# Kernel optimization log

Hardware: AMD Instinct MI355X
Metric: run time of the kernel (lower is better)

The kernel has to match this reference:

```python
import jax, jax.numpy as jnp
import numpy as np

SIGMA = 0.02
B, CC, H, W = 4, 21, 96, 96
C_LOW, C_HIGH = 3, 512
N = H * W


def _grid_edges(h, w):
    idx = np.arange(h * w).reshape(h, w)
    eh = np.stack([idx[:, :-1].ravel(), idx[:, 1:].ravel()], 1)
    ev = np.stack([idx[:-1, :].ravel(), idx[1:, :].ravel()], 1)
    return np.concatenate([eh, ev], 0)  # [E,2] 4-connected grid edges


def _mst_bfs(feat, h, w):
    # feat: [C,h,w] numpy. Kruskal MST with norm2 edge weights, then BFS from node 0.
    n = h * w
    edges = _grid_edges(h, w)
    f = feat.reshape(feat.shape[0], -1)
    wts = ((f[:, edges[:, 0]] - f[:, edges[:, 1]]) ** 2).sum(0)
    order = np.argsort(wts, kind='stable')
    uf = np.arange(n)

    def find(x):
        r = x
        while uf[r] != r:
            r = uf[r]
        while uf[x] != r:
            uf[x], x = r, uf[x]
        return r

    adj = [[] for _ in range(n)]
    cnt = 0
    for ei in order:
        a, b = int(edges[ei, 0]), int(edges[ei, 1])
        ra, rb = find(a), find(b)
        if ra != rb:
            uf[ra] = rb
            adj[a].append(b)
            adj[b].append(a)
            cnt += 1
            if cnt == n - 1:
                break
    parent = np.zeros(n, np.int64)
    seen = np.zeros(n, bool)
    seen[0] = True
    levels, frontier = [[0]], [0]
    while frontier:
        nxt = []
        for u in frontier:
            for v in adj[u]:
                if not seen[v]:
                    seen[v] = True
                    parent[v] = u
                    nxt.append(v)
        if nxt:
            levels.append(nxt)
        frontier = nxt
    return parent, levels


def _tree_arrays(embed):
    # Host-side MST + BFS level schedule (integer tree topology, non-differentiable).
    e = np.asarray(jax.device_get(embed)).astype(np.float64)
    bn = e.shape[0]
    parents, levels = [], []
    for b in range(bn):
        p, lv = _mst_bfs(e[b], H, W)
        parents.append(p)
        levels.append(lv)
    D = max(len(lv) for lv in levels)
    L = max(max(len(l) for l in lv) for lv in levels)
    nodes = np.full((bn, D, L), N, np.int32)  # index N = dummy sink node
    for b, lv in enumerate(levels):
        for d, l in enumerate(lv):
            nodes[b, d, :len(l)] = l
    par = np.stack(parents)
    par = np.concatenate([par, np.full((bn, 1), N)], 1).astype(np.int32)
    msk = np.ones((bn, N + 1), np.float32)
    msk[:, 0] = 0.0  # root has no parent edge
    msk[:, N] = 0.0  # dummy node
    return jnp.asarray(nodes), jnp.asarray(par), jnp.asarray(msk)


def _tree_filter(feat, embed, nodes, parent, wmask, sigma):
    # feat [B,C,N], embed [B,Ce,N]. O(N) two-pass (leaf->root, root->leaf) tree DP:
    # out_i = sum_j (prod_{e in path(i,j)} w_e) f_j / same-with-f=1
    bn, c, nn = feat.shape
    ez = jnp.pad(embed, ((0, 0), (0, 0), (0, 1)))  # add dummy column
    ep = jax.vmap(lambda e, p: e[:, p])(ez, parent)  # parent embedding [B,Ce,N+1]
    w = wmask * jnp.exp(-((ez - ep) ** 2).sum(1) / sigma)  # edge weight per node [B,N+1]
    fa = jnp.concatenate([feat, jnp.ones((bn, 1, nn), feat.dtype)], 1)  # append norm channel
    fa = jnp.pad(fa, ((0, 0), (0, 0), (0, 1)))  # [B,C+1,N+1]

    def one(a0, wv, par, lvls):
        def up(a, lvl):  # children before parents: subtree aggregation
            return a.at[:, par[lvl]].add(wv[lvl] * a[:, lvl]), None
        a, _ = jax.lax.scan(up, a0, lvls[::-1])

        def down(s, lvl):  # parents before children: whole-tree aggregation
            wl = wv[lvl]
            sv = a[:, lvl] + wl * (s[:, par[lvl]] - wl * a[:, lvl])
            return s.at[:, lvl].set(sv), None
        s, _ = jax.lax.scan(down, a, lvls)
        return s

    s = jax.vmap(one)(fa, w, parent, nodes)
    return s[:, :c, :nn] / s[:, c:, :nn]


def _nearest(x, h, w):
    hr, wr = x.shape[-2:]
    ri = jnp.arange(h) * hr // h
    ci = jnp.arange(w) * wr // w
    return x[..., ri[:, None], ci[None, :]]


def setup_inputs():
    key = jax.random.key(0)
    k1, k2, k3, k4 = jax.random.split(key, 4)
    preds = jax.random.normal(k1, (B, CC, H, W), jnp.float32)
    low_feats = jax.random.uniform(k2, (B, C_LOW, H, W), dtype=jnp.float32)
    high_feats = 0.03 * jax.random.normal(k3, (B, C_HIGH, H, W), jnp.float32)
    roi = (jax.random.uniform(k4, (B, 1, 2 * H, 2 * W)) > 0.5).astype(jnp.float32)
    return {'preds': preds, 'low_feats': low_feats, 'high_feats': high_feats,
            'unlabeled_ROIs': roi}


def reference(preds, low_feats, high_feats, unlabeled_ROIs):
    nodes_l, par_l, msk_l = _tree_arrays(low_feats)
    nodes_h, par_h, msk_h = _tree_arrays(high_feats)
    roi = _nearest(unlabeled_ROIs, H, W)
    n = roi.sum()
    prob = jax.nn.sigmoid(preds)
    lf = low_feats.reshape(B, C_LOW, N)
    hf = high_feats.reshape(B, C_HIGH, N)
    AS = _tree_filter(prob.reshape(B, CC, N), lf, nodes_l, par_l, msk_l, SIGMA)
    AS = _tree_filter(AS, hf, nodes_h, par_h, msk_h, 1.0)
    loss = (roi * jnp.abs(prob - AS.reshape(B, CC, H, W))).sum()
    return jnp.where(n > 0, loss / n, jnp.zeros_like(loss))
```

## Files before the change

### kernel.cpp

```cpp
#include <hip/hip_runtime.h>
#include <math.h>
#include <stdint.h>
#include <stddef.h>


namespace {
constexpr int Bn  = 4, Cc = 21, Hh = 96, Ww = 96;
constexpr int Nn  = Hh * Ww;
constexpr int EhE = Hh * (Ww - 1);
constexpr int Ne  = EhE + (Hh - 1) * Ww;
constexpr int Clow = 3, Chigh = 512;
constexpr int NCh = Cc + 1;
constexpr int MAXD = 2048;
constexpr int TL  = 2 * (Nn - 1);
constexpr int ESL = 18432;
constexpr int SEG = 19;
constexpr int NR  = (TL + SEG - 1) / SEG;
constexpr int MAXC = 4608;

constexpr size_t OFF_ACC  = 0;
constexpr size_t OFF_PROB = 256;
constexpr size_t OFF_S1   = OFF_PROB + (size_t)Bn * Cc * Nn * 4;
constexpr size_t OFF_S2   = OFF_S1   + (size_t)Bn * NCh * Nn * 4;
constexpr size_t OFF_EW   = OFF_S2   + (size_t)Bn * NCh * Nn * 4;
constexpr size_t OFF_ORD  = OFF_EW   + (size_t)8 * Ne * 8;
constexpr size_t OFF_PPOS = OFF_ORD  + (size_t)8 * Nn * 4;
constexpr size_t OFF_WGT  = OFF_PPOS + (size_t)8 * Nn * 2;
constexpr size_t OFF_LEV  = OFF_WGT  + (size_t)8 * Nn * 4;
constexpr size_t OFF_D    = OFF_LEV  + (size_t)8 * MAXD * 4;
constexpr size_t OFF_DIR  = OFF_D    + 256;
constexpr size_t OFF_CBW  = OFF_DIR  + (size_t)8 * Nn * 4;
constexpr size_t OFF_CBE  = OFF_CBW  + (size_t)8 * Nn * 8;
constexpr size_t OFF_OPP  = OFF_CBE  + (size_t)8 * Nn * 4;
constexpr size_t OFF_SGN  = OFF_OPP  + (size_t)8 * ESL * 2;
constexpr size_t OFF_PNF  = OFF_SGN  + (size_t)8 * ESL;
constexpr size_t OFF_RNK  = OFF_PNF  + (size_t)8 * Nn * 4;
constexpr size_t OFF_EL1  = OFF_ORD;
constexpr size_t OFF_EL2  = OFF_WGT;
}

__device__ __forceinline__ void edge_nodes(int e, int& a, int& b) {
    if (e < EhE) { int h = e / (Ww - 1), w = e - h * (Ww - 1); a = h * Ww + w; b = a + 1; }
    else { int e2 = e - EhE; int h = e2 / Ww, w = e2 - h * Ww; a = h * Ww + w; b = a + Ww; }
}
__device__ __forceinline__ int dir_delta(int d) {
    return (d == 0) ? 1 : (d == 1) ? -1 : (d == 2) ? Ww : -Ww;
}
__device__ __forceinline__ int edge_of(int u, int d) {
    int h = u / Ww, w = u - h * Ww;
    if (d == 0) return h * (Ww - 1) + w;
    if (d == 1) return h * (Ww - 1) + w - 1;
    if (d == 2) return EhE + u;
    return EhE + u - Ww;
}

__device__ __forceinline__ unsigned long long mkkey(double w, int e) {
    unsigned long long q = (unsigned long long)(w * 70368744177664.0);
    if (q >= (1ull << 49)) q = (1ull << 49) - 1;
    return (q << 15) | (unsigned)e;
}

__device__ __forceinline__ void compact_push(bool keep, int val, int* cnt,
                                             unsigned short* out, int lane) {
    unsigned long long m = __ballot(keep ? 1 : 0);
    if (m == 0ull) return;
    int leader = __ffsll((unsigned long long)m) - 1;
    int base = 0;
    if (lane == leader) base = atomicAdd(cnt, __popcll(m));
    base = __shfl(base, leader, 64);
    if (keep) {
        unsigned long long lower = m & ((1ull << lane) - 1ull);
        out[base + __popcll(lower)] = (unsigned short)val;
    }
}

__device__ __forceinline__ int scan1024s(int val, int tid, int* wsum) {
    __syncthreads();
    int lane = tid & 63, wv = tid >> 6;
    int x = val;
    #pragma unroll
    for (int off = 1; off < 64; off <<= 1) {
        int y = __shfl_up(x, off, 64);
        if (lane >= off) x += y;
    }
    if (lane == 63) wsum[wv] = x;
    __syncthreads();
    if (wv == 0) {
        int s2 = (lane < 16) ? wsum[lane] : 0;
        #pragma unroll
        for (int off = 1; off < 16; off <<= 1) {
            int y = __shfl_up(s2, off, 64);
            if (lane >= off) s2 += y;
        }
        if (lane < 16) wsum[lane] = s2;
    }
    __syncthreads();
    int base = (wv > 0) ? wsum[wv - 1] : 0;
    return x + base;
}

__device__ __forceinline__ int scan1024_incl(int val, int tid, int* b0, int* b1) {
    b0[tid] = val;
    __syncthreads();
    int* s = b0; int* d = b1;
    for (int off = 1; off < 1024; off <<= 1) {
        int x = s[tid];
        if (tid >= off) x += s[tid - off];
        d[tid] = x;
        __syncthreads();
        int* t = s; s = d; d = t;
    }
    return s[tid];
}

__global__ void k_init(const float* __restrict__ preds, float* __restrict__ prob,
                       double* __restrict__ acc) {
    int idx = blockIdx.x * blockDim.x + threadIdx.x;
    if (idx == 0) { acc[0] = 0.0; acc[1] = 0.0; }
    if (idx >= Bn * Cc * Nn) return;
    prob[idx] = 1.0f / (1.0f + expf(-preds[idx]));
}

__global__ void k_edgew(const float* __restrict__ feat, int C, double* __restrict__ ew) {
    int idx = blockIdx.x * blockDim.x + threadIdx.x;
    if (idx >= Bn * Ne) return;
    int b = idx / Ne, e = idx - b * Ne;
    int a, c2; edge_nodes(e, a, c2);
    const float* fa = feat + (size_t)b * C * Nn + a;
    const float* fb = feat + (size_t)b * C * Nn + c2;
    double s = 0.0;
    int c = 0;
    for (; c + 16 <= C; c += 16) {
        float va[16], vb[16];
        #pragma unroll
        for (int k = 0; k < 16; k++) {
            va[k] = fa[(size_t)(c + k) * Nn];
            vb[k] = fb[(size_t)(c + k) * Nn];
        }
        #pragma unroll
        for (int k = 0; k < 16; k++) {
            double d = (double)va[k] - (double)vb[k];
            s += d * d;
        }
    }
    for (; c < C; c++) {
        double d = (double)fa[(size_t)c * Nn] - (double)fb[(size_t)c * Nn];
        s += d * d;
    }
    ew[idx] = s;
}

__global__ void __launch_bounds__(1024)
k_mst(char* __restrict__ ws) {
    const int tb = blockIdx.x, tid = threadIdx.x;
    const int lane = tid & 63;
    const double* ew = (const double*)(ws + OFF_EW) + (size_t)tb * Ne;
    int* dirG = (int*)(ws + OFF_DIR) + (size_t)tb * Nn;
    unsigned short* elA = (unsigned short*)(ws + OFF_EL1) + (size_t)tb * Ne;
    unsigned short* elB = (unsigned short*)(ws + OFF_EL2) + (size_t)tb * Ne;

    __shared__ unsigned short comp[Nn];
    __shared__ unsigned long long cbK[MAXC];
    __shared__ int scanBuf[2048];
    __shared__ int chgArr[48];
    __shared__ int sLen, sNC;

    unsigned short* nxtN     = (unsigned short*)cbK;
    unsigned short* newSlotN = (unsigned short*)cbK + Nn;
    unsigned short* nxt      = (unsigned short*)cbK;
    unsigned short* newSlot  = (unsigned short*)cbK + MAXC;

    for (int i = tid; i < Nn; i += 1024) dirG[i] = 0;
    if (tid < 48) chgArr[tid] = 0;
    __syncthreads();

    for (int i = tid; i < Nn; i += 1024) {
        int h = i / Ww, w = i - h * Ww;
        unsigned long long bk = ~0ull;
        if (w < Ww - 1) { int e = h * (Ww - 1) + w;     unsigned long long k = mkkey(ew[e], e); if (k < bk) bk = k; }
        if (w > 0)      { int e = h * (Ww - 1) + w - 1; unsigned long long k = mkkey(ew[e], e); if (k < bk) bk = k; }
        if (h < Hh - 1) { int e = EhE + i;              unsigned long long k = mkkey(ew[e], e); if (k < bk) bk = k; }
        if (h > 0)      { int e = EhE + i - Ww;         unsigned long long k = mkkey(ew[e], e); if (k < bk) bk = k; }
        int e = (int)(bk & 0x7FFF);
        int a, c; edge_nodes(e, a, c);
        nxtN[i] = (unsigned short)((a == i) ? c : a);
        int da = (c == a + 1) ? 0 : 2;
        atomicOr(&dirG[a], 1 << da);
        atomicOr(&dirG[c], 1 << (da ^ 1));
    }
    __syncthreads();
    for (int i = tid; i < Nn; i += 1024) {
        int o = nxtN[i];
        if (o != i && nxtN[o] == i && i < o) nxtN[i] = (unsigned short)i;
    }
    __syncthreads();
    {
        int it = 0;
        while (it < 40) {
            bool any = false;
            for (int r = tid; r < Nn; r += 1024) {
                int nr = nxtN[r], nnr = nxtN[nr];
                if (nr != nnr) { nxtN[r] = (unsigned short)nnr; any = true; }
            }
            if (any) chgArr[it] = 1;
            __syncthreads();
            if (!chgArr[it]) break;
            it++;
        }
    }
    {
        int base = tid * 9, cnt = 0, loc[9];
        #pragma unroll
        for (int k = 0; k < 9; k++) {
            int i = base + k;
            loc[k] = cnt;
            if (nxtN[i] == i) cnt++;
        }
        int incl = scan1024_incl(cnt, tid, scanBuf, scanBuf + 1024);
        int eb = incl - cnt;
        #pragma unroll
        for (int k = 0; k < 9; k++) {
            int i = base + k;
            if (nxtN[i] == i) newSlotN[i] = (unsigned short)(eb + loc[k]);
        }
        if (tid == 1023) sNC = incl;
    }
    __syncthreads();
    for (int i = tid; i < Nn; i += 1024) comp[i] = newSlotN[nxtN[i]];
    __syncthreads();
    int nComp = sNC;

    unsigned short* src = elA;
    unsigned short* dst = elB;
    int srcLen = -1;
    for (int round = 2; round < 22 && nComp > 1; round++) {
        if (tid == 0) sLen = 0;
        if (tid < 48) chgArr[tid] = 0;
        __syncthreads();
        if (srcLen < 0) {
            for (int e = tid; e < Ne; e += 1024) {
                int a, c; edge_nodes(e, a, c);
                compact_push(comp[a] != comp[c], e, &sLen, dst, lane);
            }
        } else {
            for (int k = tid; k < srcLen; k += 1024) {
                int e = src[k];
                int a, c; edge_nodes(e, a, c);
                compact_push(comp[a] != comp[c], e, &sLen, dst, lane);
            }
        }
        for (int s = tid; s < nComp; s += 1024) cbK[s] = ~0ull;
        __syncthreads();
        int len = sLen;
        if (len == 0) break;
        for (int k = tid; k < len; k += 1024) {
            int e = dst[k];
            int a, c; edge_nodes(e, a, c);
            unsigned long long key = mkkey(ew[e], e);
            atomicMin(&cbK[comp[a]], key);
            atomicMin(&cbK[comp[c]], key);
        }
        __syncthreads();
        unsigned long long kr[5];
        int nOwn = 0;
        for (int s = tid; s < nComp; s += 1024) kr[nOwn++] = cbK[s];
        __syncthreads();
        {
            int o = 0;
            for (int s = tid; s < nComp; s += 1024, o++) {
                unsigned long long key = kr[o];
                if (key != ~0ull) {
                    int e = (int)(key & 0x7FFF);
                    int a, c; edge_nodes(e, a, c);
                    int sa = comp[a], sc = comp[c];
                    nxt[s] = (unsigned short)((sa == s) ? sc : sa);
                    int da = (c == a + 1) ? 0 : 2;
                    atomicOr(&dirG[a], 1 << da);
                    atomicOr(&dirG[c], 1 << (da ^ 1));
                } else nxt[s] = (unsigned short)s;
            }
        }
        __syncthreads();
        for (int s = tid; s < nComp; s += 1024) {
            int o = nxt[s];
            if (o != s && nxt[o] == s && s < o) nxt[s] = (unsigned short)s;
        }
        __syncthreads();
        {
            int it = 0;
            while (it < 40) {
                bool any = false;
                for (int s = tid; s < nComp; s += 1024) {
                    int ns = nxt[s], nns = nxt[ns];
                    if (ns != nns) { nxt[s] = (unsigned short)nns; any = true; }
                }
                if (any) chgArr[it] = 1;
                __syncthreads();
                if (!chgArr[it]) break;
                it++;
            }
        }
        {
            int K = (nComp + 1023) >> 10;
            int base = tid * K, cnt = 0, loc[5];
            for (int k = 0; k < K; k++) {
                int s = base + k;
                loc[k] = cnt;
                if (s < nComp && nxt[s] == s) cnt++;
            }
            int incl = scan1024_incl(cnt, tid, scanBuf, scanBuf + 1024);
            int eb = incl - cnt;
            for (int k = 0; k < K; k++) {
                int s = base + k;
                if (s < nComp && nxt[s] == s) newSlot[s] = (unsigned short)(eb + loc[k]);
            }
            if (tid == 1023) sNC = incl;
        }
        __syncthreads();
        for (int i = tid; i < Nn; i += 1024) comp[i] = newSlot[nxt[comp[i]]];
        __syncthreads();
        nComp = sNC;
        unsigned short* t = src; src = dst; dst = t;
        srcLen = len;
    }
}

__global__ void __launch_bounds__(1024)
k_topo(char* __restrict__ ws) {
    const int tb = blockIdx.x, tid = threadIdx.x;
    const int lane = tid & 63, wv = tid >> 6;
    const int tree = tb >> 2;
    const double* ew  = (const double*)(ws + OFF_EW) + (size_t)tb * Ne;
    const int*  dirG  = (const int*)(ws + OFF_DIR) + (size_t)tb * Nn;
    unsigned int*   elemSegG = (unsigned int*)(ws + OFF_CBW + (size_t)tb * 73728);
    unsigned short* ORG      = (unsigned short*)(ws + OFF_CBW + (size_t)tb * 73728);
    unsigned short* OWNR     = ORG + ESL;
    unsigned short* ownG     = (unsigned short*)(ws + OFF_CBE + (size_t)tb * (size_t)ESL * 2);
    unsigned short* oppG     = (unsigned short*)(ws + OFF_OPP + (size_t)tb * (size_t)ESL * 2);
    unsigned short* IRG      = (unsigned short*)(ws + OFF_SGN + (size_t)tb * ESL);
    unsigned short* rank0G   = (unsigned short*)(ws + OFF_RNK + (size_t)tb * (size_t)ESL * 2);
    int*            ordG  = (int*)(ws + OFF_ORD)  + (size_t)tb * Nn;
    unsigned short* pposG = (unsigned short*)(ws + OFF_PPOS) + (size_t)tb * Nn;
    float*          wgtG  = (float*)(ws + OFF_WGT) + (size_t)tb * Nn;
    int*            levG  = (int*)(ws + OFF_LEV)  + (size_t)tb * MAXD;
    int*            dG    = (int*)(ws + OFF_D);
    const float inv_sigma = tree ? 1.0f : 50.0f;

    __shared__ char A[36864];
    __shared__ char B[18432];
    __shared__ char C[9216];
    __shared__ int  wsum[16];
    __shared__ int  sR, sPack, sCenter;

    unsigned short* degOff = (unsigned short*)B;
    unsigned char*  nbS    = (unsigned char*)C;
    for (int i = tid; i < Nn; i += 1024) nbS[i] = (unsigned char)dirG[i];
    __syncthreads();
    {
        int base9 = tid * 9;
        int loc[9]; int s = 0;
        #pragma unroll
        for (int k = 0; k < 9; k++) { loc[k] = s; s += __popc(nbS[base9 + k]); }
        int incl = scan1024s(s, tid, wsum);
        int eb = incl - s;
        #pragma unroll
        for (int k = 0; k < 9; k++) degOff[base9 + k] = (unsigned short)(eb + loc[k]);
    }
    __syncthreads();

    unsigned short* nxtS = (unsigned short*)A;
    for (int u = tid; u < Nn; u += 1024) {
        int m = nbS[u]; int base = degOff[u]; int k = 0;
        #pragma unroll
        for (int d = 0; d < 4; d++) {
            if (m & (1 << d)) {
                int v = u + dir_delta(d);
                int mv = nbS[v]; int rd = d ^ 1;
                int pv = __popc(mv & ((1 << rd) - 1));
                int dv = __popc(mv);
                int nx = pv + 1; if (nx == dv) nx = 0;
                int j = base + k;
                nxtS[j] = (unsigned short)(degOff[v] + nx);
                ownG[j] = (unsigned short)((u << 2) | d);
                oppG[j] = (unsigned short)(degOff[v] + pv);
                k++;
            }
        }
    }
    __syncthreads();

    int myNr = 0, myLen = 0;
    if (tid < NR) {
        int x = tid * SEG, off = 0;
        for (int g = 0; g < 4096; g++) {
            elemSegG[x] = ((unsigned)tid << 11) | (unsigned)off;
            int y = nxtS[x];
            if (y % SEG == 0) { myNr = y / SEG; myLen = off + 1; break; }
            x = y; off++;
        }
    }
    __syncthreads();

    unsigned short* cn  = (unsigned short*)C;
    unsigned short* cd  = (unsigned short*)(C + 2048);
    unsigned short* nn2 = (unsigned short*)(C + 4096);
    unsigned short* nd2 = (unsigned short*)(C + 6144);
    if (tid == 0)      { cn[0] = 0; cd[0] = 0; }
    else if (tid < NR) { cn[tid] = (unsigned short)myNr; cd[tid] = (unsigned short)myLen; }
    else               { cn[tid] = (unsigned short)tid; cd[tid] = 0; }
    __syncthreads();
    for (int r = 0; r < 10; r++) {
        int c = cn[tid];
        int dv = cd[tid] + cd[c];
        int n2 = cn[c];
        nn2[tid] = (unsigned short)n2; nd2[tid] = (unsigned short)dv;
        __syncthreads();
        unsigned short* t;
        t = cn; cn = nn2; nn2 = t;
        t = cd; cd = nd2; nd2 = t;
    }
    unsigned short* rb = nn2;
    rb[tid] = (tid == 0) ? 0 : (unsigned short)(TL - cd[tid]);
    __syncthreads();

    for (int hh = 0; hh < 2; hh++) {
        unsigned int pk4[9];
        #pragma unroll
        for (int t = 0; t < 9; t++) {
            int e = tid + (hh * 9 + t) * 1024;
            pk4[t] = elemSegG[e < TL ? e : 0];
        }
        unsigned short rbv[9];
        #pragma unroll
        for (int t = 0; t < 9; t++) rbv[t] = rb[pk4[t] >> 11];
        #pragma unroll
        for (int t = 0; t < 9; t++) {
            int e = tid + (hh * 9 + t) * 1024;
            if (e < TL) rank0G[e] = (unsigned short)(rbv[t] + (pk4[t] & 2047));
        }
    }
    __syncthreads();

    for (int hh = 0; hh < 2; hh++) {
        unsigned short rnk[9], opp[9], own2[9];
        #pragma unroll
        for (int t = 0; t < 9; t++) {
            int j = tid + (hh * 9 + t) * 1024;
            int ja = j < TL ? j : 0;
            rnk[t] = rank0G[ja]; opp[t] = oppG[ja]; own2[t] = ownG[ja];
        }
        unsigned short r2[9];
        #pragma unroll
        for (int t = 0; t < 9; t++) r2[t] = rank0G[opp[t]];
        #pragma unroll
        for (int t = 0; t < 9; t++) {
            int j = tid + (hh * 9 + t) * 1024;
            if (j < TL) { int r = rnk[t]; ORG[r] = r2[t]; OWNR[r] = own2[t]; }
        }
    }
    {
        unsigned short dof[9];
        #pragma unroll
        for (int t = 0; t < 9; t++) dof[t] = degOff[tid + t * 1024];
        unsigned short ov[9];
        #pragma unroll
        for (int t = 0; t < 9; t++) ov[t] = oppG[dof[t]];
        unsigned short rv[9];
        #pragma unroll
        for (int t = 0; t < 9; t++) rv[t] = rank0G[ov[t]];
        #pragma unroll
        for (int t = 0; t < 9; t++) IRG[tid + t * 1024] = rv[t];
    }
    __syncthreads();

    short* scanS = (short*)A;
    unsigned char* parC = (unsigned char*)C;
    unsigned short* depthB = (unsigned short*)B;
    int curRoot = 0, rootC = 0;
    for (int ph = 0; ph < 3; ph++) {
        if (tid == 0) {
            sR = ORG[IRG[curRoot]];
            sPack = 0;
        }
        __syncthreads();
        const int R = sR;
        const bool doPar = (ph >= 1);
        int base = tid * 18;
        int n = TL - base; if (n > 18) n = 18; if (n < 0) n = 0;
        unsigned short orvA[18], ownA[18];
        #pragma unroll
        for (int k = 0; k < 18; k++) {
            int q = base + k;
            int r = q + R; if (r >= TL) r -= TL; if (q >= TL) r = 0;
            orvA[k] = ORG[r];
        }
        if (doPar) {
            #pragma unroll
            for (int k = 0; k < 18; k++) {
                int q = base + k;
                int r = q + R; if (r >= TL) r -= TL; if (q >= TL) r = 0;
                ownA[k] = OWNR[r];
            }
        }
        short loc[18]; int s = 0;
        #pragma unroll
        for (int k = 0; k < 18; k++) {
            if (k < n) {
                int q = base + k;
                int rro = (int)orvA[k] - R; if (rro < 0) rro += TL;
                bool desc = q < rro;
                if (doPar && desc) {
                    int own = ownA[k];
                    int head = (own >> 2) + dir_delta(own & 3);
                    parC[head] = (unsigned char)((own & 3) ^ 1);
                }
                s += desc ? 1 : -1;
                loc[k] = (short)s;
            }
        }
        int incl = scan1024s(s, tid, wsum);
        int eb = incl - s;
        #pragma unroll
        for (int k = 0; k < 18; k++)
            if (k < n) scanS[base + k] = (short)(loc[k] + eb);
        __syncthreads();
        int pk = 0;
        {
            unsigned short qA[9];
            #pragma unroll
            for (int j = 0; j < 9; j++) qA[j] = IRG[tid + j * 1024];
            int depA[9];
            #pragma unroll
            for (int j = 0; j < 9; j++) {
                int q = (int)qA[j] - R; if (q < 0) q += TL;
                depA[j] = (int)scanS[q];
            }
            #pragma unroll
            for (int j = 0; j < 9; j++) {
                int x = tid + j * 1024;
                int dep = (x == curRoot) ? 0 : depA[j];
                int p2 = (dep << 14) | x;
                if (p2 > pk) pk = p2;
                if (ph == 2) depthB[x] = (unsigned short)dep;
            }
        }
        #pragma unroll
        for (int off = 32; off > 0; off >>= 1) {
            int o = __shfl_down(pk, off, 64);
            if (o > pk) pk = o;
        }
        if (lane == 0) atomicMax(&sPack, pk);
        __syncthreads();
        if (ph == 0) curRoot = sPack & 16383;
        else if (ph == 1) {
            int diam = sPack >> 14, v = sPack & 16383;
            int steps = diam - (diam >> 1);
            unsigned short* J  = (unsigned short*)A;
            unsigned short* J2 = (unsigned short*)(A + 18432);
            for (int x = tid; x < Nn; x += 1024)
                J[x] = (unsigned short)((x == curRoot) ? x : (x + dir_delta(parC[x])));
            if (tid == 0) sCenter = v;
            __syncthreads();
            for (int k = 0; (steps >> k) != 0; k++) {
                if (tid == 0 && ((steps >> k) & 1)) sCenter = J[sCenter];
                if ((steps >> (k + 1)) != 0) {
                    __syncthreads();
                    for (int x = tid; x < Nn; x += 1024) J2[x] = J[J[x]];
                    __syncthreads();
                    unsigned short* t = J; J = J2; J2 = t;
                }
            }
            __syncthreads();
            curRoot = sCenter;
            rootC = curRoot;
        }
        __syncthreads();
    }
    const int D = (sPack >> 14) + 1;

    unsigned short* posOf = (unsigned short*)A;
    int* hist   = (int*)(A + 18432);
    int* levOff = (int*)(A + 26624);
    for (int k = tid; k < 2048; k += 1024) hist[k] = 0;
    __syncthreads();
    for (int v = tid; v < Nn; v += 1024) atomicAdd(&hist[depthB[v]], 1);
    __syncthreads();
    {
        int h0 = hist[2 * tid], h1 = hist[2 * tid + 1];
        int partial = h0 + h1;
        int incl = scan1024s(partial, tid, wsum);
        int eb = incl - partial;
        levOff[2 * tid] = eb;
        levOff[2 * tid + 1] = eb + h0;
    }
    __syncthreads();
    for (int d = tid; d <= D && d < 2048; d += 1024) levG[d] = levOff[d];
    for (int k = tid; k < 2048; k += 1024) hist[k] = 0;
    __syncthreads();
    for (int v = tid; v < Nn; v += 1024) {
        int dep = depthB[v];
        int pos = levOff[dep] + atomicAdd(&hist[dep], 1);
        posOf[v] = (unsigned short)pos;
        ordG[pos] = v;
    }
    __syncthreads();

    {
        unsigned char rdA[9]; unsigned short posA[9];
        #pragma unroll
        for (int t = 0; t < 9; t++) {
            int v = tid + t * 1024;
            rdA[t] = parC[v]; posA[t] = posOf[v];
        }
        double ewv[9]; unsigned short ppv[9];
        #pragma unroll
        for (int t = 0; t < 9; t++) {
            int v = tid + t * 1024;
            int rd = rdA[t] & 3;
            bool ir = (v == rootC);
            int p  = ir ? v : v + dir_delta(rd);
            int ei = ir ? 0 : edge_of(v, rd);
            ppv[t] = posOf[p];
            ewv[t] = ew[ei];
        }
        #pragma unroll
        for (int t = 0; t < 9; t++) {
            int v = tid + t * 1024;
            int pos = posA[t];
            if (v == rootC) { pposG[pos] = 0; wgtG[pos] = 0.0f; }
            else {
                pposG[pos] = ppv[t];
                wgtG[pos] = expf(-(float)ewv[t] * inv_sigma);
            }
        }
    }
    if (tid == 0) dG[tb] = D;
}

__global__ void __launch_bounds__(64)
k_dp(char* __restrict__ ws, int tree, int inMode) {
    const int bc = blockIdx.x;
    const int b = bc / NCh, c = bc % NCh;
    const int tb = tree * Bn + b;
    const int lane = threadIdx.x;
    const int*            ordG  = (const int*)(ws + OFF_ORD)  + (size_t)tb * Nn;
    const unsigned short* pposG = (const unsigned short*)(ws + OFF_PPOS) + (size_t)tb * Nn;
    const float*          wgtG  = (const float*)(ws + OFF_WGT) + (size_t)tb * Nn;
    const int*            levG  = (const int*)(ws + OFF_LEV)  + (size_t)tb * MAXD;
    const int D = ((const int*)(ws + OFF_D))[tb];
    const float* src = (inMode == 0)
        ? (const float*)(ws + OFF_PROB) + ((size_t)b * Cc + c) * Nn
        : (const float*)(ws + OFF_S1)   + ((size_t)b * NCh + c) * Nn;
    const float* srcN = (const float*)(ws + OFF_S1) + ((size_t)b * NCh + Cc) * Nn;
    float* dst = (float*)(ws + (tree ? OFF_S2 : OFF_S1)) + ((size_t)b * NCh + c) * Nn;

    __shared__ alignas(16) float Al[Nn];
    __shared__ alignas(16) float wgtS[Nn];
    __shared__ alignas(16) unsigned short pposS[Nn];
    __shared__ unsigned short levS[MAXD];

    {
        const uint4* pg4 = (const uint4*)pposG;
        uint4* ps4 = (uint4*)pposS;
        for (int k = lane; k < Nn / 8; k += 64) ps4[k] = pg4[k];
        const uint4* wg4 = (const uint4*)wgtG;
        uint4* ws4 = (uint4*)wgtS;
        for (int k = lane; k < Nn / 4; k += 64) ws4[k] = wg4[k];
    }
    for (int d = lane; d <= D && d < MAXD; d += 64) levS[d] = (unsigned short)levG[d];
    if (c == Cc)            { for (int i = lane; i < Nn; i += 64) Al[i] = 1.0f; }
    else if (inMode == 0)   { for (int i = lane; i < Nn; i += 64) Al[i] = src[ordG[i]]; }
    else                    { for (int i = lane; i < Nn; i += 64) { int nd = ordG[i]; Al[i] = src[nd] / srcN[nd]; } }
    __builtin_amdgcn_wave_barrier();
    asm volatile("" ::: "memory");

    if (D > 1) {
        int sd = levS[D - 1], sd1 = levS[D];
        for (int d = D - 1; d >= 1; d--) {
            int nb = (d > 1) ? (int)levS[d - 1] : 0;
            for (int i = sd + lane; i < sd1; i += 64)
                atomicAdd(&Al[pposS[i]], wgtS[i] * Al[i]);
            __builtin_amdgcn_wave_barrier();
            asm volatile("" ::: "memory");
            sd1 = sd; sd = nb;
        }
    }
    if (D > 1) {
        int sd = levS[1], sd1 = levS[2];
        for (int d = 1; d < D; d++) {
            int nb = (d + 2 <= D) ? (int)levS[d + 2] : 0;
            for (int i = sd + lane; i < sd1; i += 64) {
                float w = wgtS[i], a = Al[i];
                Al[i] = a + w * (Al[pposS[i]] - w * a);
            }
            __builtin_amdgcn_wave_barrier();
            asm volatile("" ::: "memory");
            sd = sd1; sd1 = nb;
        }
    }
    __builtin_amdgcn_wave_barrier();
    asm volatile("" ::: "memory");
    for (int i = lane; i < Nn; i += 64) dst[ordG[i]] = Al[i];
}

__global__ void k_loss(char* __restrict__ ws, const float* __restrict__ roi) {
    const int tid = threadIdx.x;
    int idx = blockIdx.x * 256 + tid;
    const float* prob = (const float*)(ws + OFF_PROB);
    const float* S2   = (const float*)(ws + OFF_S2);
    double* acc = (double*)(ws + OFF_ACC);
    double ls = 0.0, cnt = 0.0;
    if (idx < Bn * Cc * Nn) {
        int b = idx / (Cc * Nn);
        int rem = idx - b * (Cc * Nn);
        int c = rem / Nn, n = rem - c * Nn;
        int h = n / Ww, w2 = n - h * Ww;
        float r = roi[(size_t)b * (2 * Hh) * (2 * Ww) + (size_t)(2 * h) * (2 * Ww) + 2 * w2];
        float as = S2[((size_t)b * NCh + c) * Nn + n] / S2[((size_t)b * NCh + Cc) * Nn + n];
        float pp = prob[((size_t)b * Cc + c) * Nn + n];
        ls = (double)(r * fabsf(pp - as));
        if (c == 0) cnt = (double)r;
    }
    __shared__ double sl[256], sc2[256];
    sl[tid] = ls; sc2[tid] = cnt;
    __syncthreads();
    for (int s = 128; s > 0; s >>= 1) {
        if (tid < s) { sl[tid] += sl[tid + s]; sc2[tid] += sc2[tid + s]; }
        __syncthreads();
    }
    if (tid == 0) { atomicAdd(acc, sl[0]); atomicAdd(acc + 1, sc2[0]); }
}

__global__ void k_final(const double* __restrict__ acc, float* __restrict__ out) {
    if (blockIdx.x == 0 && threadIdx.x == 0)
        out[0] = (acc[1] > 0.0) ? (float)(acc[0] / acc[1]) : 0.0f;
}

extern "C" void kernel_launch(void* const* d_in, const int* in_sizes, int n_in,
                              void* d_out, int out_size, void* d_ws, size_t ws_size,
                              hipStream_t stream) {
    const float* preds = (const float*)d_in[0];
    const float* lowf  = (const float*)d_in[1];
    const float* highf = (const float*)d_in[2];
    const float* roi   = (const float*)d_in[3];
    char* ws = (char*)d_ws;
    float* out = (float*)d_out;
    double* ewl = (double*)(ws + OFF_EW);
    double* ewh = (double*)(ws + OFF_EW) + (size_t)Bn * Ne;

    k_init<<<(Bn * Cc * Nn + 255) / 256, 256, 0, stream>>>(
        preds, (float*)(ws + OFF_PROB), (double*)(ws + OFF_ACC));
    k_edgew<<<(Bn * Ne + 255) / 256, 256, 0, stream>>>(lowf, Clow, ewl);
    k_edgew<<<(Bn * Ne + 255) / 256, 256, 0, stream>>>(highf, Chigh, ewh);
    k_mst<<<8, 1024, 0, stream>>>(ws);
    k_topo<<<8, 1024, 0, stream>>>(ws);
    k_dp<<<Bn * NCh, 64, 0, stream>>>(ws, 0, 0);
    k_dp<<<Bn * NCh, 64, 0, stream>>>(ws, 1, 1);
    k_loss<<<(Bn * Cc * Nn + 255) / 256, 256, 0, stream>>>(ws, roi);
    k_final<<<1, 64, 0, stream>>>((const double*)(ws + OFF_ACC), out);
}
```

Measured before the change: 670.1 us.

## Replace BFS level schedule with heavy-path decomposition in tree DP

Topology construction now computes subtree sizes, picks heavy children, and decomposes each MST into heavy paths grouped by light-edge depth. Paths are laid out contiguously, and the DP kernel processes each path serially per lane, one batch of paths at a time. This replaces one wave barrier per BFS level, across a tree depth that can reach thousands of levels, with a number of batches bounded by the light depth. In exchange the topology kernel does more work (pointer jumping, prefix scans), and lanes in a batch have unbalanced serial path lengths. The layout also assumes path counts fit in PMAX and light depths stay small.

```diff
diff --git a/kernel.cpp b/kernel.cpp
--- a/kernel.cpp
+++ b/kernel.cpp
@@ -17,6 +17,8 @@
 constexpr int SEG = 19;
 constexpr int NR  = (TL + SEG - 1) / SEG;
 constexpr int MAXC = 4608;
+constexpr int PMAX = 6176;
+constexpr size_t PTAB = (size_t)10 * PMAX * 2;
 
 constexpr size_t OFF_ACC  = 0;
 constexpr size_t OFF_PROB = 256;
@@ -35,6 +37,10 @@
 constexpr size_t OFF_SGN  = OFF_OPP  + (size_t)8 * ESL * 2;
 constexpr size_t OFF_PNF  = OFF_SGN  + (size_t)8 * ESL;
 constexpr size_t OFF_RNK  = OFF_PNF  + (size_t)8 * Nn * 4;
+constexpr size_t OFF_SZ   = OFF_RNK  + (size_t)8 * ESL * 2;
+constexpr size_t OFF_HPID = OFF_SZ   + (size_t)8 * Nn * 2;
+constexpr size_t OFF_PTA  = OFF_HPID + (size_t)8 * Nn * 2;
+constexpr size_t OFF_BOF  = OFF_PTA  + (size_t)8 * PTAB;
 constexpr size_t OFF_EL1  = OFF_ORD;
 constexpr size_t OFF_EL2  = OFF_WGT;
 }
@@ -340,10 +346,23 @@
     unsigned short* IRG      = (unsigned short*)(ws + OFF_SGN + (size_t)tb * ESL);
     unsigned short* rank0G   = (unsigned short*)(ws + OFF_RNK + (size_t)tb * (size_t)ESL * 2);
     int*            ordG  = (int*)(ws + OFF_ORD)  + (size_t)tb * Nn;
-    unsigned short* pposG = (unsigned short*)(ws + OFF_PPOS) + (size_t)tb * Nn;
     float*          wgtG  = (float*)(ws + OFF_WGT) + (size_t)tb * Nn;
-    int*            levG  = (int*)(ws + OFF_LEV)  + (size_t)tb * MAXD;
     int*            dG    = (int*)(ws + OFF_D);
+    unsigned short* sizeGp = (unsigned short*)(ws + OFF_SZ) + (size_t)tb * Nn;
+    unsigned short* hIdxG  = (unsigned short*)(ws + OFF_HPID) + (size_t)tb * Nn;
+    unsigned short* ptaT   = (unsigned short*)(ws + OFF_PTA + (size_t)tb * PTAB);
+    unsigned short* hlistU = ptaT;
+    unsigned short* lenU   = ptaT + PMAX;
+    unsigned short* ancA   = ptaT + 2 * PMAX;
+    unsigned short* btA    = ptaT + 3 * PMAX;
+    unsigned short* ancB   = ptaT + 4 * PMAX;
+    unsigned short* btB    = ptaT + 5 * PMAX;
+    unsigned short* pLs    = ptaT + 6 * PMAX;
+    unsigned short* pHh    = ptaT + 7 * PMAX;
+    unsigned short* pSs    = ptaT + 8 * PMAX;
+    unsigned short* pHpp   = ptaT + 9 * PMAX;
+    int* iScr = (int*)(ptaT + 6 * PMAX);
+    int* bofG = (int*)(ws + OFF_BOF) + tb * 64;
     const float inv_sigma = tree ? 1.0f : 50.0f;
 
     __shared__ char A[36864];
@@ -351,10 +370,12 @@
     __shared__ char C[9216];
     __shared__ int  wsum[16];
     __shared__ int  sR, sPack, sCenter;
+    __shared__ int  cA2[64];
 
     unsigned short* degOff = (unsigned short*)B;
     unsigned char*  nbS    = (unsigned char*)C;
     for (int i = tid; i < Nn; i += 1024) nbS[i] = (unsigned char)dirG[i];
+    if (tid < 64) cA2[tid] = 0;
     __syncthreads();
     {
         int base9 = tid * 9;
@@ -513,6 +534,8 @@
                     int own = ownA[k];
                     int head = (own >> 2) + dir_delta(own & 3);
                     parC[head] = (unsigned char)((own & 3) ^ 1);
+                    if (ph == 2)
+                        sizeGp[head] = (unsigned short)((rro - q + 1) >> 1);
                 }
                 s += desc ? 1 : -1;
                 loc[k] = (short)s;
@@ -578,61 +601,134 @@
     }
     const int D = (sPack >> 14) + 1;
 
-    unsigned short* posOf = (unsigned short*)A;
-    int* hist   = (int*)(A + 18432);
-    int* levOff = (int*)(A + 26624);
-    for (int k = tid; k < 2048; k += 1024) hist[k] = 0;
-    __syncthreads();
-    for (int v = tid; v < Nn; v += 1024) atomicAdd(&hist[depthB[v]], 1);
-    __syncthreads();
+    unsigned char*  heavyA = (unsigned char*)A;
+    unsigned short* J1     = (unsigned short*)A;
+    unsigned short* hdA    = (unsigned short*)(A + 18432);
+
+    for (int v = tid; v < Nn; v += 1024) {
+        int h = v / Ww, w = v - h * Ww;
+        int best = 0, hv = 4;
+        if (w < Ww - 1) { int u = v + 1;  if (u != rootC && parC[u] == 1) { int sz = sizeGp[u]; if (sz > best) { best = sz; hv = 0; } } }
+        if (w > 0)      { int u = v - 1;  if (u != rootC && parC[u] == 0) { int sz = sizeGp[u]; if (sz > best) { best = sz; hv = 1; } } }
+        if (h < Hh - 1) { int u = v + Ww; if (u != rootC && parC[u] == 3) { int sz = sizeGp[u]; if (sz > best) { best = sz; hv = 2; } } }
+        if (h > 0)      { int u = v - Ww; if (u != rootC && parC[u] == 2) { int sz = sizeGp[u]; if (sz > best) { best = sz; hv = 3; } } }
+        heavyA[v] = (unsigned char)hv;
+    }
+    __syncthreads();
+    for (int v = tid; v < Nn; v += 1024) {
+        bool ih; int p = 0;
+        if (v == rootC) ih = true;
+        else { p = v + dir_delta(parC[v]); ih = (heavyA[p] != (parC[v] ^ 1)); }
+        hdA[v] = (unsigned short)(ih ? v : p);
+        if (ih) {
+            int hi = atomicAdd(&cA2[0], 1);
+            hlistU[hi] = (unsigned short)v;
+            hIdxG[v] = (unsigned short)hi;
+        }
+    }
+    __syncthreads();
+    const int nP = cA2[0];
     {
-        int h0 = hist[2 * tid], h1 = hist[2 * tid + 1];
-        int partial = h0 + h1;
-        int incl = scan1024s(partial, tid, wsum);
-        int eb = incl - partial;
-        levOff[2 * tid] = eb;
-        levOff[2 * tid + 1] = eb + h0;
-    }
-    __syncthreads();
-    for (int d = tid; d <= D && d < 2048; d += 1024) levG[d] = levOff[d];
-    for (int k = tid; k < 2048; k += 1024) hist[k] = 0;
+        unsigned short* cur = hdA;
+        unsigned short* nxt = J1;
+        for (int r = 0; r < 12; r++) {
+            for (int v = tid; v < Nn; v += 1024) nxt[v] = cur[cur[v]];
+            __syncthreads();
+            unsigned short* t = cur; cur = nxt; nxt = t;
+        }
+    }
+    for (int k = tid; k < nP; k += 1024) iScr[k] = 0;
     __syncthreads();
     for (int v = tid; v < Nn; v += 1024) {
-        int dep = depthB[v];
-        int pos = levOff[dep] + atomicAdd(&hist[dep], 1);
-        posOf[v] = (unsigned short)pos;
+        int hd = hdA[v];
+        atomicMax(&iScr[hIdxG[hd]], (int)depthB[v] - (int)depthB[hd] + 1);
+    }
+    __syncthreads();
+    for (int k = tid; k < nP; k += 1024) {
+        int h = hlistU[k];
+        if (h == rootC) { ancA[k] = (unsigned short)k; btA[k] = 0; }
+        else {
+            int p = h + dir_delta(parC[h]);
+            ancA[k] = hIdxG[hdA[p]];
+            btA[k] = 1;
+        }
+    }
+    __syncthreads();
+    for (int r = 0; r < 5; r++) {
+        for (int k = tid; k < nP; k += 1024) {
+            int a = ancA[k];
+            btB[k] = (unsigned short)(btA[k] + btA[a]);
+            ancB[k] = ancA[a];
+        }
+        __syncthreads();
+        unsigned short* t;
+        t = ancA; ancA = ancB; ancB = t;
+        t = btA;  btA  = btB;  btB  = t;
+    }
+    for (int k = tid; k < nP; k += 1024) lenU[k] = (unsigned short)iScr[k];
+    __syncthreads();
+    for (int k = tid; k < nP; k += 1024) {
+        int bt2 = btA[k];
+        atomicAdd(&cA2[8 + bt2], 1);
+        atomicMax(&cA2[1], bt2);
+    }
+    __syncthreads();
+    if (tid == 0) {
+        int nb2 = cA2[1] + 1;
+        int acc = 0;
+        bofG[0] = nb2;
+        for (int i2 = 0; i2 < nb2; i2++) {
+            int t2 = cA2[8 + i2];
+            cA2[8 + i2] = acc;
+            bofG[1 + i2] = acc;
+            acc += t2;
+        }
+        bofG[1 + nb2] = acc;
+    }
+    __syncthreads();
+    for (int k = tid; k < nP; k += 1024) {
+        int pid = atomicAdd(&cA2[8 + btA[k]], 1);
+        pLs[pid] = lenU[k];
+        pHh[pid] = hlistU[k];
+        hIdxG[hlistU[k]] = (unsigned short)pid;
+    }
+    __syncthreads();
+    {
+        int base7 = tid * 7;
+        int loc7[7]; int s = 0;
+        #pragma unroll
+        for (int k = 0; k < 7; k++) {
+            int idx = base7 + k;
+            loc7[k] = s;
+            s += (idx < nP) ? (int)pLs[idx] : 0;
+        }
+        int incl = scan1024s(s, tid, wsum);
+        int eb = incl - s;
+        #pragma unroll
+        for (int k = 0; k < 7; k++) {
+            int idx = base7 + k;
+            if (idx < nP) pSs[idx] = (unsigned short)(eb + loc7[k]);
+        }
+    }
+    __syncthreads();
+    for (int k = tid; k < nP; k += 1024) {
+        int h = pHh[k];
+        unsigned short hpp = 0xFFFF;
+        if (h != rootC) {
+            int p = h + dir_delta(parC[h]);
+            int hp = hdA[p];
+            hpp = (unsigned short)((int)pSs[hIdxG[hp]] + (int)depthB[p] - (int)depthB[hp]);
+        }
+        pHpp[k] = hpp;
+    }
+    __syncthreads();
+    for (int v = tid; v < Nn; v += 1024) {
+        int hdv = hdA[v];
+        int pid = hIdxG[hdv];
+        int pos = (int)pSs[pid] + (int)depthB[v] - (int)depthB[hdv];
         ordG[pos] = v;
-    }
-    __syncthreads();
-
-    {
-        unsigned char rdA[9]; unsigned short posA[9];
-        #pragma unroll
-        for (int t = 0; t < 9; t++) {
-            int v = tid + t * 1024;
-            rdA[t] = parC[v]; posA[t] = posOf[v];
-        }
-        double ewv[9]; unsigned short ppv[9];
-        #pragma unroll
-        for (int t = 0; t < 9; t++) {
-            int v = tid + t * 1024;
-            int rd = rdA[t] & 3;
-            bool ir = (v == rootC);
-            int p  = ir ? v : v + dir_delta(rd);
-            int ei = ir ? 0 : edge_of(v, rd);
-            ppv[t] = posOf[p];
-            ewv[t] = ew[ei];
-        }
-        #pragma unroll
-        for (int t = 0; t < 9; t++) {
-            int v = tid + t * 1024;
-            int pos = posA[t];
-            if (v == rootC) { pposG[pos] = 0; wgtG[pos] = 0.0f; }
-            else {
-                pposG[pos] = ppv[t];
-                wgtG[pos] = expf(-(float)ewv[t] * inv_sigma);
-            }
-        }
+        wgtG[pos] = (v == rootC) ? 0.0f
+                  : expf(-(float)ew[edge_of(v, parC[v])] * inv_sigma);
     }
     if (tid == 0) dG[tb] = D;
 }
@@ -643,11 +739,13 @@
     const int b = bc / NCh, c = bc % NCh;
     const int tb = tree * Bn + b;
     const int lane = threadIdx.x;
-    const int*            ordG  = (const int*)(ws + OFF_ORD)  + (size_t)tb * Nn;
-    const unsigned short* pposG = (const unsigned short*)(ws + OFF_PPOS) + (size_t)tb * Nn;
-    const float*          wgtG  = (const float*)(ws + OFF_WGT) + (size_t)tb * Nn;
-    const int*            levG  = (const int*)(ws + OFF_LEV)  + (size_t)tb * MAXD;
-    const int D = ((const int*)(ws + OFF_D))[tb];
+    const int*   ordG = (const int*)(ws + OFF_ORD) + (size_t)tb * Nn;
+    const float* wgtG = (const float*)(ws + OFF_WGT) + (size_t)tb * Nn;
+    const unsigned short* ptaT = (const unsigned short*)(ws + OFF_PTA + (size_t)tb * PTAB);
+    const unsigned short* pLsG = ptaT + 6 * PMAX;
+    const unsigned short* pSsG = ptaT + 8 * PMAX;
+    const unsigned short* pHpG = ptaT + 9 * PMAX;
+    const int* bofG = (const int*)(ws + OFF_BOF) + tb * 64;
     const float* src = (inMode == 0)
         ? (const float*)(ws + OFF_PROB) + ((size_t)b * Cc + c) * Nn
         : (const float*)(ws + OFF_S1)   + ((size_t)b * NCh + c) * Nn;
@@ -656,46 +754,81 @@
 
     __shared__ alignas(16) float Al[Nn];
     __shared__ alignas(16) float wgtS[Nn];
-    __shared__ alignas(16) unsigned short pposS[Nn];
-    __shared__ unsigned short levS[MAXD];
-
+    __shared__ unsigned short pS[PMAX], pL[PMAX], pH[PMAX];
+    __shared__ int bOff[40];
+
+    const int nb = bofG[0];
+    const int nP = bofG[1 + nb];
+    for (int k = lane; k <= nb; k += 64) bOff[k] = bofG[1 + k];
+    for (int k = lane; k < nP; k += 64) {
+        pS[k] = pSsG[k]; pL[k] = pLsG[k]; pH[k] = pHpG[k];
+    }
     {
-        const uint4* pg4 = (const uint4*)pposG;
-        uint4* ps4 = (uint4*)pposS;
-        for (int k = lane; k < Nn / 8; k += 64) ps4[k] = pg4[k];
         const uint4* wg4 = (const uint4*)wgtG;
         uint4* ws4 = (uint4*)wgtS;
         for (int k = lane; k < Nn / 4; k += 64) ws4[k] = wg4[k];
     }
-    for (int d = lane; d <= D && d < MAXD; d += 64) levS[d] = (unsigned short)levG[d];
     if (c == Cc)            { for (int i = lane; i < Nn; i += 64) Al[i] = 1.0f; }
     else if (inMode == 0)   { for (int i = lane; i < Nn; i += 64) Al[i] = src[ordG[i]]; }
     else                    { for (int i = lane; i < Nn; i += 64) { int nd = ordG[i]; Al[i] = src[nd] / srcN[nd]; } }
     __builtin_amdgcn_wave_barrier();
     asm volatile("" ::: "memory");
 
-    if (D > 1) {
-        int sd = levS[D - 1], sd1 = levS[D];
-        for (int d = D - 1; d >= 1; d--) {
-            int nb = (d > 1) ? (int)levS[d - 1] : 0;
-            for (int i = sd + lane; i < sd1; i += 64)
-                atomicAdd(&Al[pposS[i]], wgtS[i] * Al[i]);
+    for (int bb = nb - 1; bb >= 0; bb--) {
+        int base = bOff[bb], cnt = bOff[bb + 1] - base;
+        for (int c0 = 0; c0 < cnt; c0 += 64) {
+            int idx = c0 + lane;
+            if (idx < cnt) {
+                int pid = base + idx;
+                int ps = pS[pid], len = pL[pid], hpp = pH[pid];
+                int i = ps + len - 1;
+                float u = Al[i];
+                i--;
+                while (i - 3 >= ps) {
+                    float A0 = Al[i], A1 = Al[i-1], A2 = Al[i-2], A3 = Al[i-3];
+                    float W0 = wgtS[i+1], W1 = wgtS[i], W2 = wgtS[i-1], W3 = wgtS[i-2];
+                    u = A0 + W0 * u; Al[i]   = u;
+                    u = A1 + W1 * u; Al[i-1] = u;
+                    u = A2 + W2 * u; Al[i-2] = u;
+                    u = A3 + W3 * u; Al[i-3] = u;
+                    i -= 4;
+                }
+                while (i >= ps) { u = Al[i] + wgtS[i+1] * u; Al[i] = u; i--; }
+                if (hpp != 0xFFFF) atomicAdd(&Al[hpp], wgtS[ps] * u);
+            }
             __builtin_amdgcn_wave_barrier();
             asm volatile("" ::: "memory");
-            sd1 = sd; sd = nb;
-        }
-    }
-    if (D > 1) {
-        int sd = levS[1], sd1 = levS[2];
-        for (int d = 1; d < D; d++) {
-            int nb = (d + 2 <= D) ? (int)levS[d + 2] : 0;
-            for (int i = sd + lane; i < sd1; i += 64) {
-                float w = wgtS[i], a = Al[i];
-                Al[i] = a + w * (Al[pposS[i]] - w * a);
+        }
+    }
+    __builtin_amdgcn_wave_barrier();
+    asm volatile("" ::: "memory");
+    for (int bb = 0; bb < nb; bb++) {
+        int base = bOff[bb], cnt = bOff[bb + 1] - base;
+        for (int c0 = 0; c0 < cnt; c0 += 64) {
+            int idx = c0 + lane;
+            if (idx < cnt) {
+                int pid = base + idx;
+                int ps = pS[pid], len = pL[pid], hpp = pH[pid];
+                int i = ps, end = ps + len;
+                float sp;
+                if (hpp == 0xFFFF) { sp = Al[i]; i++; }
+                else sp = Al[hpp];
+                while (i + 3 < end) {
+                    float A0 = Al[i], A1 = Al[i+1], A2 = Al[i+2], A3 = Al[i+3];
+                    float W0 = wgtS[i], W1 = wgtS[i+1], W2 = wgtS[i+2], W3 = wgtS[i+3];
+                    sp = A0 + W0 * (sp - W0 * A0); Al[i]   = sp;
+                    sp = A1 + W1 * (sp - W1 * A1); Al[i+1] = sp;
+                    sp = A2 + W2 * (sp - W2 * A2); Al[i+2] = sp;
+                    sp = A3 + W3 * (sp - W3 * A3); Al[i+3] = sp;
+                    i += 4;
+                }
+                while (i < end) {
+                    float w = wgtS[i], a = Al[i];
+                    sp = a + w * (sp - w * a); Al[i] = sp; i++;
+                }
             }
             __builtin_amdgcn_wave_barrier();
             asm volatile("" ::: "memory");
-            sd = sd1; sd1 = nb;
         }
     }
     __builtin_amdgcn_wave_barrier();
```

Result: slower. 778.1 us (+16.1%).
